# Optimization experiments

Hardware: AMD Instinct MI355X
Metric: run time of the kernel (lower is better)

## Reference

```python
import jax, jax.numpy as jnp
import numpy as np

N = 50000      # nodes
E = 800000     # edges (avg degree 16)
IN = 128       # in_feats
OUT = 128      # out_feats
ASSIGN = 256   # assign_dim = B graphs * 8 clusters
B = 32         # batch_size (num graphs)


def setup_inputs() -> dict:
    key = jax.random.key(0)
    k0, k1, k2, k3 = jax.random.split(key, 4)
    x = jax.random.normal(k0, (N, IN), jnp.float32)
    edge_index = jax.random.randint(k1, (2, E), 0, N, dtype=jnp.int32)
    # sorted graph ids, ~equal-sized graphs (mirrors block_diag mask construction)
    batch = ((jnp.arange(N, dtype=jnp.int32) * B) // N).astype(jnp.int32)
    # SAGEConv params: Linear(2*in_feats -> out) on concat([x, mean_neigh])
    W_embed = jax.random.normal(k2, (2 * IN, OUT), jnp.float32) / np.float32(np.sqrt(2 * IN))
    b_embed = jnp.zeros((OUT,), jnp.float32)
    W_pool = jax.random.normal(k3, (2 * IN, ASSIGN), jnp.float32) / np.float32(np.sqrt(2 * IN))
    b_pool = jnp.zeros((ASSIGN,), jnp.float32)
    return dict(x=x, edge_index=edge_index, batch=batch,
                W_embed=W_embed, b_embed=b_embed, W_pool=W_pool, b_pool=b_pool)


def _sage(x, src, dst, W, b):
    # mean aggregation over in-neighbors (messages src -> dst), then Linear on concat
    n = x.shape[0]
    deg = jax.ops.segment_sum(jnp.ones((src.shape[0],), x.dtype), dst, num_segments=n)
    neigh = jax.ops.segment_sum(x[src], dst, num_segments=n) / jnp.maximum(deg, 1.0)[:, None]
    return jnp.concatenate([x, neigh], axis=-1) @ W + b


def reference(x, edge_index, batch, W_embed, b_embed, W_pool, b_pool):
    src, dst = edge_index[0], edge_index[1]
    embed = _sage(x, src, dst, W_embed, b_embed)                      # [N, OUT]
    pooled = jax.nn.softmax(_sage(x, src, dst, W_pool, b_pool), -1)   # [N, ASSIGN]
    # block-diagonal mask: node i of graph g sees columns [g*C, (g+1)*C)
    C = ASSIGN // B
    cols = jnp.arange(ASSIGN, dtype=batch.dtype) // C
    mask = (batch[:, None] == cols[None, :]).astype(x.dtype)          # [N, ASSIGN]
    # NOTE: faithful to original: softmax of (mask * pooled), zeros contribute exp(0)
    r = jax.nn.softmax(mask * pooled, axis=-1) * mask
    r = r / (r.sum(axis=-1, keepdims=True) + 1e-13)                   # [N, ASSIGN]
    h = r.T @ embed                                                   # [ASSIGN, OUT]
    # adj_new = S^T A S with A sparse COO (rows=edge_index[0], cols=edge_index[1])
    ar = jax.ops.segment_sum(r[dst], src, num_segments=x.shape[0])    # A @ S : [N, ASSIGN]
    adj_new = r.T @ ar                                                # [ASSIGN, ASSIGN]
    return (adj_new, h)
```

## Files before the change

### kernel.cpp

```cpp
#include <hip/hip_runtime.h>
#include <hip/hip_bf16.h>

#define N_ 50000
#define E_ 800000
#define IN_ 128
#define OUT_ 128
#define ASSIGN_ 256
#define B_ 32
#define KTOT 256
#define JTOT 384
#define HCHUNK 32
#define ACHUNK 32
#define AST 72
#define NXP ((N_ + 127) / 128)
#define NGB (NXP * 3)
#define NCVX 6250

#define NBKT 256
#define NPB 196
#define BCAP 4000
#define EPB 4096
#define NBLK_A ((E_ + EPB - 1) / EPB)
#define NPRE (NBLK_A + NCVX + 384)

typedef __attribute__((ext_vector_type(8))) short short8;
typedef __attribute__((ext_vector_type(4))) float f32x4;
typedef __attribute__((ext_vector_type(2))) float f32x2;
typedef __attribute__((ext_vector_type(4))) unsigned short ushort4v;
typedef __attribute__((ext_vector_type(2))) unsigned short ushort2v;
typedef unsigned short u16;

__device__ inline unsigned short f2bf(float v) {
    union { float f; unsigned u; } a;
    a.f = v;
    unsigned r = a.u + 0x7fff + ((a.u >> 16) & 1);
    return (unsigned short)(r >> 16);
}
__device__ inline float bf2f(unsigned short b) {
    union { unsigned u; float f; } a;
    a.u = ((unsigned)b) << 16;
    return a.f;
}

__device__ inline unsigned enc8(float v) {
    union { float f; unsigned u; } a;
    a.f = v * 0x1p-120f;
    unsigned b = a.u;
    unsigned r = b + 0x7FFFF + ((b >> 20) & 1);
    return ((r >> 20) & 0x7F) | ((b >> 24) & 0x80);
}
__device__ inline float2 dec8x2(unsigned short p) {
#if defined(__has_builtin) && __has_builtin(__builtin_amdgcn_cvt_pk_f32_fp8)
    f32x2 r = __builtin_amdgcn_cvt_pk_f32_fp8((int)(unsigned)p, false);
    return make_float2(r.x, r.y);
#else
    unsigned u0 = p & 0xffu, u1 = (p >> 8) & 0xffu;
    union { unsigned u; float f; } a, b;
    a.u = ((u0 & 0x80u) << 24) | ((u0 & 0x7fu) << 20);
    b.u = ((u1 & 0x80u) << 24) | ((u1 & 0x7fu) << 20);
    return make_float2(a.f * 0x1p+120f, b.f * 0x1p+120f);
#endif
}

__global__ __launch_bounds__(256) void k_pre(const int* __restrict__ ei,
                                             int* __restrict__ bktFill,
                                             int2* __restrict__ ebkt,
                                             const float* __restrict__ x,
                                             unsigned short* __restrict__ xhi,
                                             unsigned char* __restrict__ xq,
                                             const float* __restrict__ We,
                                             const float* __restrict__ be,
                                             const float* __restrict__ Wp,
                                             const float* __restrict__ bp,
                                             unsigned short* __restrict__ WThi,
                                             float* __restrict__ bias) {
    __shared__ int lh[NBKT], lbase[NBKT], lofs[NBKT];
    int bid = blockIdx.x;
    int t = threadIdx.x;
    if (bid < NBLK_A) {
        int e0 = bid * EPB;
        lh[t] = 0; lofs[t] = 0;
        __syncthreads();
        int ss[16], dd[16];
#pragma unroll
        for (int i = 0; i < 16; i++) {
            int e = e0 + i * 256 + t;
            ss[i] = 0; dd[i] = -1;
            if (e < E_) {
                ss[i] = ei[e];
                dd[i] = ei[E_ + e];
                atomicAdd(&lh[dd[i] / NPB], 1);
            }
        }
        __syncthreads();
        lbase[t] = t * BCAP + atomicAdd(&bktFill[t], lh[t]);
        __syncthreads();
#pragma unroll
        for (int i = 0; i < 16; i++) {
            if (dd[i] >= 0) {
                int b = dd[i] / NPB;
                int o = atomicAdd(&lofs[b], 1);
                ebkt[lbase[b] + o] = make_int2(ss[i], dd[i]);
            }
        }
        return;
    }
    if (bid >= NBLK_A + NCVX) {
        int idx = (bid - NBLK_A - NCVX) * 256 + t;
        if (idx < JTOT * KTOT) {
            int j = idx / KTOT, k = idx - j * KTOT;
            float v = (j < 128) ? We[k * 128 + j] : Wp[k * 256 + (j - 128)];
            WThi[idx] = f2bf(v);
        }
        if (idx < JTOT) bias[idx] = (idx < 128) ? be[idx] : bp[idx - 128];
        return;
    }
    int i4 = ((bid - NBLK_A) * 256 + t) * 4;
    if (i4 >= N_ * 128) return;
    float4 v = *(const float4*)(x + i4);
    ushort4v h;
    h.x = f2bf(v.x); h.y = f2bf(v.y); h.z = f2bf(v.z); h.w = f2bf(v.w);
    *(ushort4v*)(xhi + i4) = h;
    unsigned q = enc8(v.x) | (enc8(v.y) << 8) | (enc8(v.z) << 16) | (enc8(v.w) << 24);
    *(unsigned*)(xq + i4) = q;
}

__global__ __launch_bounds__(256) void k_binB(const int* __restrict__ bktFill,
                                              const int2* __restrict__ ebkt,
                                              int* __restrict__ ready,
                                              int* __restrict__ rowStart,
                                              int* __restrict__ csr_src,
                                              int* __restrict__ csr_dst) {
    __shared__ int ldeg[NPB];
    __shared__ int lscan[256];
    __shared__ int bsc[NBKT];
    __shared__ int lfill[NPB];
    int b = blockIdx.x, t = threadIdx.x;
    if (t < NPB) ldeg[t] = 0;
    __syncthreads();
    int base = b * BCAP;
    int cnt = bktFill[b];
    int n0 = b * NPB;
    for (int j = t; j < cnt; j += 256)
        atomicAdd(&ldeg[ebkt[base + j].y - n0], 1);
    __syncthreads();
    lscan[t] = (t < NPB) ? ldeg[t] : 0;
    __syncthreads();
    for (int off = 1; off < 256; off <<= 1) {
        int x0 = lscan[t];
        int a0 = (t >= off) ? lscan[t - off] : 0;
        __syncthreads();
        lscan[t] = x0 + a0;
        __syncthreads();
    }
    if (t == 0) atomicExch(&ready[b], lscan[NPB - 1] + 1);
    {
        int v;
        while ((v = atomicAdd(&ready[t], 0)) == 0) __builtin_amdgcn_s_sleep(8);
        bsc[t] = v - 1;
    }
    __syncthreads();
    for (int off = 1; off < NBKT; off <<= 1) {
        int x = bsc[t];
        int add = (t >= off) ? bsc[t - off] : 0;
        __syncthreads();
        bsc[t] = x + add;
        __syncthreads();
    }
    int base0 = (b == 0) ? 0 : bsc[b - 1];
    if (t < NPB) {
        int n = n0 + t;
        if (n < N_) {
            int excl = (t == 0) ? 0 : lscan[t - 1];
            lfill[t] = excl;
            rowStart[n] = base0 + excl;
        }
    }
    __syncthreads();
    for (int j = t; j < cnt; j += 256) {
        int2 sd = ebkt[base + j];
        int p = base0 + atomicAdd(&lfill[sd.y - n0], 1);
        csr_src[p] = sd.x;
        csr_dst[p] = sd.y;
    }
    if (b == 0 && t == 0) rowStart[N_] = E_;
}

__global__ __launch_bounds__(256) void k_agg(const unsigned char* __restrict__ xq,
                                             const int* __restrict__ rowStart,
                                             const int* __restrict__ csr_src,
                                             unsigned short* __restrict__ nhi) {
    int node = blockIdx.x * 4 + (threadIdx.x >> 6);
    if (node >= N_) return;
    int lane = threadIdx.x & 63;
    int es = lane >> 3;
    int fb = lane & 7;
    int a = rowStart[node], bnd = rowStart[node + 1];
    float acc[16];
#pragma unroll
    for (int k = 0; k < 16; k++) acc[k] = 0.f;
#define DEC(Q)                                                       \
    {                                                                \
        unsigned wq[4] = {(Q).x, (Q).y, (Q).z, (Q).w};               \
        _Pragma("unroll")                                            \
        for (int wi = 0; wi < 4; wi++) {                             \
            float2 f01 = dec8x2((unsigned short)(wq[wi] & 0xffffu)); \
            float2 f23 = dec8x2((unsigned short)(wq[wi] >> 16));     \
            acc[wi * 4 + 0] += f01.x; acc[wi * 4 + 1] += f01.y;      \
            acc[wi * 4 + 2] += f23.x; acc[wi * 4 + 3] += f23.y;      \
        }                                                            \
    }
    int j = a;
    for (; j + 8 < bnd; j += 16) {
        int s0 = csr_src[j + es];
        uint4 q0 = *(const uint4*)(xq + (size_t)s0 * 128 + fb * 16);
        uint4 q1 = {0, 0, 0, 0};
        int e1 = j + 8 + es;
        if (e1 < bnd) {
            int s1 = csr_src[e1];
            q1 = *(const uint4*)(xq + (size_t)s1 * 128 + fb * 16);
        }
        DEC(q0);
        DEC(q1);
    }
    if (j < bnd) {
        uint4 q0 = {0, 0, 0, 0};
        int e0 = j + es;
        if (e0 < bnd) {
            int s0 = csr_src[e0];
            q0 = *(const uint4*)(xq + (size_t)s0 * 128 + fb * 16);
        }
        DEC(q0);
    }
#undef DEC
#pragma unroll
    for (int k = 0; k < 16; k++) {
        acc[k] += __shfl_xor(acc[k], 8, 64);
        acc[k] += __shfl_xor(acc[k], 16, 64);
        acc[k] += __shfl_xor(acc[k], 32, 64);
    }
    float inv = 1.0f / (float)max(bnd - a, 1);
    if (es == 0) {
        short8 o0, o1;
#pragma unroll
        for (int k = 0; k < 8; k++) {
            o0[k] = (short)f2bf(acc[k] * inv);
            o1[k] = (short)f2bf(acc[k + 8] * inv);
        }
        *(short8*)(nhi + (size_t)node * 128 + fb * 16) = o0;
        *(short8*)(nhi + (size_t)node * 128 + fb * 16 + 8) = o1;
    }
}

#define LDA 40
__global__ __launch_bounds__(256) void k_gemm(const unsigned short* __restrict__ xhi,
                                              const unsigned short* __restrict__ nhi,
                                              const unsigned short* __restrict__ WThi,
                                              const float* __restrict__ bias,
                                              unsigned short* __restrict__ embed,
                                              unsigned short* __restrict__ plog) {
    __shared__ __align__(16) union {
        struct { u16 Ah[128][LDA]; u16 Bh[128][LDA]; } s;
        u16 ep[64 * 128];
    } sm;
    int t = threadIdx.x;
    int wave = t >> 6, lane = t & 63;
    int wm = wave >> 1, wn = wave & 1;
    int q = lane >> 4, lr = lane & 15;

    int id = blockIdx.x;
    int xi, cc;
    if (id < (NXP / 8) * 24) {
        xi = (id / 24) * 8 + (id & 7);
        cc = (id % 24) >> 3;
    } else {
        int r2 = id - (NXP / 8) * 24;
        xi = (NXP / 8) * 8 + r2 % (NXP % 8);
        cc = r2 / (NXP % 8);
    }
    int row0 = xi * 128;
    int col0 = cc * 128;

    f32x4 acc[4][4] = {};
    int smr = t >> 1;
    int kc = (t & 1) * 16;
    int node = row0 + smr;

    short8 vh0, vh1, wh0, wh1;
#define LOADK(KT)                                                                    \
    {                                                                                \
        const u16* Ah_src = ((KT) < 128) ? xhi : nhi;                                \
        int kb = ((KT) & 127) + kc;                                                  \
        vh0 = {}; vh1 = {};                                                          \
        if (node < N_) {                                                             \
            const short8* ph = (const short8*)(Ah_src + (size_t)node * 128 + kb);    \
            vh0 = ph[0]; vh1 = ph[1];                                                \
        }                                                                            \
        const short8* pw = (const short8*)(WThi + (size_t)(col0 + smr) * 256 + (KT) + kc); \
        wh0 = pw[0]; wh1 = pw[1];                                                    \
    }
    LOADK(0);
    for (int kt = 0; kt < KTOT; kt += 32) {
        *(short8*)&sm.s.Ah[smr][kc] = vh0;
        *(short8*)&sm.s.Ah[smr][kc + 8] = vh1;
        *(short8*)&sm.s.Bh[smr][kc] = wh0;
        *(short8*)&sm.s.Bh[smr][kc + 8] = wh1;
        __syncthreads();
        if (kt + 32 < KTOT) LOADK(kt + 32);

        short8 afh[4];
#pragma unroll
        for (int mi = 0; mi < 4; mi++) {
            int r = wm * 64 + mi * 16 + lr;
            afh[mi] = *(const short8*)&sm.s.Ah[r][q * 8];
        }
#pragma unroll
        for (int ni = 0; ni < 4; ni++) {
            int r = wn * 64 + ni * 16 + lr;
            short8 bfh = *(const short8*)&sm.s.Bh[r][q * 8];
#pragma unroll
            for (int mi = 0; mi < 4; mi++)
                acc[mi][ni] = __builtin_amdgcn_mfma_f32_16x16x32_bf16(afh[mi], bfh, acc[mi][ni], 0, 0, 0);
        }
        __syncthreads();
    }
#undef LOADK

    for (int half = 0; half < 2; half++) {
        __syncthreads();
        if (wm == half) {
#pragma unroll
            for (int mi = 0; mi < 4; mi++)
#pragma unroll
                for (int ni = 0; ni < 4; ni++) {
                    int lcol = wn * 64 + ni * 16 + lr;
                    float bj = bias[col0 + lcol];
#pragma unroll
                    for (int r = 0; r < 4; r++) {
                        int lrow = mi * 16 + q * 4 + r;
                        sm.ep[lrow * 128 + lcol] = f2bf(acc[mi][ni][r] + bj);
                    }
                }
        }
        __syncthreads();
#pragma unroll
        for (int i = 0; i < 4; i++) {
            int chunk = i * 256 + t;
            int lrow = chunk >> 4;
            int lco = (chunk & 15) * 8;
            int grow = row0 + half * 64 + lrow;
            if (grow < N_) {
                short8 v = *(const short8*)&sm.ep[lrow * 128 + lco];
                if (col0 < 128)
                    *(short8*)(embed + (size_t)grow * 128 + lco) = v;
                else
                    *(short8*)(plog + (size_t)grow * 256 + (col0 - 128) + lco) = v;
            }
        }
    }
}

__global__ __launch_bounds__(256) void k_r(const unsigned short* __restrict__ plog,
                                           const int* __restrict__ batch,
                                           float* __restrict__ r8,
                                           unsigned short* __restrict__ r8b) {
    int node = blockIdx.x * 4 + (threadIdx.x >> 6);
    int lane = threadIdx.x & 63;
    if (node >= N_) return;
    ushort4v p4 = *(const ushort4v*)(plog + (size_t)node * 256 + lane * 4);
    float px = bf2f(p4.x), py = bf2f(p4.y), pz = bf2f(p4.z), pw = bf2f(p4.w);
    float m = fmaxf(fmaxf(px, py), fmaxf(pz, pw));
    for (int off = 32; off; off >>= 1) m = fmaxf(m, __shfl_xor(m, off, 64));
    float s = expf(px - m) + expf(py - m) + expf(pz - m) + expf(pw - m);
    for (int off = 32; off; off >>= 1) s += __shfl_xor(s, off, 64);
    int g = batch[node];
    float v = 0.f;
    if (lane < 8) v = expf(bf2f(plog[(size_t)node * 256 + g * 8 + lane]) - m) / s;
    float M2 = v;
    for (int off = 4; off; off >>= 1) M2 = fmaxf(M2, __shfl_xor(M2, off, 64));
    float e = expf(v - M2);
    float Sg = e;
    for (int off = 4; off; off >>= 1) Sg += __shfl_xor(Sg, off, 64);
    float D2 = Sg + 248.0f * expf(-M2);
    float r = e / (Sg + 1e-13f * D2);
    if (lane < 8) {
        r8[node * 8 + lane] = r;
        r8b[node * 8 + lane] = f2bf(r);
    }
}

__global__ __launch_bounds__(256) void k_tail(const int* __restrict__ rowStart,
                                              const int* __restrict__ csr_src,
                                              const int* __restrict__ csr_dst,
                                              const unsigned short* __restrict__ r8b,
                                              float* __restrict__ partAdj,
                                              const unsigned short* __restrict__ embed,
                                              const float* __restrict__ r8,
                                              float* __restrict__ partH) {
    __shared__ __align__(16) unsigned short Ab[256 * AST];
    __shared__ __align__(16) unsigned short Bb[16 * AST];
    int id = blockIdx.x;
    int t = threadIdx.x;
    if (id >= B_ * ACHUNK) {
        int idh = id - B_ * ACHUNK;
        int g = idh & 31;
        int c = idh >> 5;
        int wv = t >> 6, l = t & 63;
        int n0g = (g * N_ + 31) >> 5;
        int n1g = ((g + 1) * N_ + 31) >> 5;
        int len = n1g - n0g;
        int a = n0g + (len * c) / HCHUNK;
        int b = n0g + (len * (c + 1)) / HCHUNK;
        float acc[8][2] = {};
        for (int n = a + wv; n < b; n += 4) {
            unsigned e2 = *(const unsigned*)(embed + (size_t)n * 128 + l * 2);
            float e0 = bf2f((u16)(e2 & 0xffffu));
            float e1 = bf2f((u16)(e2 >> 16));
            f32x4 r0 = *(const f32x4*)(r8 + n * 8);
            f32x4 r1 = *(const f32x4*)(r8 + n * 8 + 4);
#pragma unroll
            for (int c2 = 0; c2 < 4; c2++) {
                acc[c2][0] += r0[c2] * e0; acc[c2][1] += r0[c2] * e1;
                acc[c2 + 4][0] += r1[c2] * e0; acc[c2 + 4][1] += r1[c2] * e1;
            }
        }
        float* hredf = (float*)Ab;
#pragma unroll
        for (int c2 = 0; c2 < 8; c2++) {
            hredf[wv * 1024 + c2 * 128 + l * 2] = acc[c2][0];
            hredf[wv * 1024 + c2 * 128 + l * 2 + 1] = acc[c2][1];
        }
        __syncthreads();
        float* pb = partH + (g * HCHUNK + c) * 1024;
        for (int o = t; o < 1024; o += 256)
            pb[o] = (hredf[o] + hredf[1024 + o]) + (hredf[2048 + o] + hredf[3072 + o]);
        return;
    }
    int gd = id & 31;
    int c = id >> 5;
    int wave = t >> 6, lane = t & 63;
    int q = lane >> 4, lr = lane & 15;
    int n0g = (gd * N_ + 31) >> 5;
    int n1g = ((gd + 1) * N_ + 31) >> 5;
    int len = n1g - n0g;
    int na = n0g + (len * c) / ACHUNK;
    int nb = n0g + (len * (c + 1)) / ACHUNK;
    int j0 = rowStart[na], j1 = rowStart[nb];

    uint4 z = {0, 0, 0, 0};
#pragma unroll
    for (int i = 0; i < 9; i++) *(uint4*)&Ab[(i * 256 + t) * 8] = z;
    if (t < 144) *(uint4*)&Bb[t * 8] = z;
    __syncthreads();

    f32x4 acc[4] = {};
    int el = t >> 2;
    int ap = t & 3;

    int jcur = j0 + el;
    unsigned sv = 0, dv = 0;
    int gs = 0;
    bool have = jcur < j1;
    if (have) {
        int s = csr_src[jcur];
        int d = csr_dst[jcur];
        gs = (s * B_) / N_;
        sv = *(const unsigned*)(r8b + (size_t)s * 8 + ap * 2);
        dv = *(const unsigned*)(r8b + (size_t)d * 8 + ap * 2);
    }
    int pca = -1;

    for (int jt = j0; jt < j1; jt += 64) {
        if (pca >= 0) {
            Ab[pca * AST + el] = 0;
            Ab[(pca + 1) * AST + el] = 0;
            Bb[(ap * 2) * AST + el] = 0;
            Bb[(ap * 2 + 1) * AST + el] = 0;
        }
        int ca = -1;
        if (have) {
            ca = gs * 8 + ap * 2;
            Ab[ca * AST + el] = (unsigned short)sv;
            Ab[(ca + 1) * AST + el] = (unsigned short)(sv >> 16);
            Bb[(ap * 2) * AST + el] = (unsigned short)dv;
            Bb[(ap * 2 + 1) * AST + el] = (unsigned short)(dv >> 16);
        }
        __syncthreads();
        int jn = jt + 64 + el;
        bool haveN = jn < j1;
        unsigned svN = 0, dvN = 0;
        int gsN = 0;
        if (haveN) {
            int s = csr_src[jn];
            int d = csr_dst[jn];
            gsN = (s * B_) / N_;
            svN = *(const unsigned*)(r8b + (size_t)s * 8 + ap * 2);
            dvN = *(const unsigned*)(r8b + (size_t)d * 8 + ap * 2);
        }
        short8 bf0 = *(const short8*)&Bb[lr * AST + q * 8];
        short8 bf1 = *(const short8*)&Bb[lr * AST + 32 + q * 8];
#pragma unroll
        for (int mi = 0; mi < 4; mi++) {
            int col = (wave * 4 + mi) * 16 + lr;
            short8 a0 = *(const short8*)&Ab[col * AST + q * 8];
            short8 a1 = *(const short8*)&Ab[col * AST + 32 + q * 8];
            acc[mi] = __builtin_amdgcn_mfma_f32_16x16x32_bf16(a0, bf0, acc[mi], 0, 0, 0);
            acc[mi] = __builtin_amdgcn_mfma_f32_16x16x32_bf16(a1, bf1, acc[mi], 0, 0, 0);
        }
        __syncthreads();
        pca = ca;
        have = haveN; gs = gsN; sv = svN; dv = dvN;
    }

    float* pb = partAdj + (gd * ACHUNK + c) * 2048;
    if (lr < 8) {
#pragma unroll
        for (int mi = 0; mi < 4; mi++) {
            int mbase = (wave * 4 + mi) * 16 + q * 4;
#pragma unroll
            for (int r = 0; r < 4; r++)
                pb[(mbase + r) * 8 + lr] = acc[mi][r];
        }
    }
}

__global__ __launch_bounds__(256) void k_red(const float* __restrict__ partAdj,
                                             const float* __restrict__ partH,
                                             float* __restrict__ out) {
    int o = blockIdx.x * 256 + threadIdx.x;
    if (o < 256 * 256) {
        int row = o >> 8, col = o & 255;
        int gd = col >> 3, b = col & 7;
        int li = row * 8 + b;
        float s = 0.f;
#pragma unroll
        for (int c = 0; c < ACHUNK; c++) s += partAdj[(gd * ACHUNK + c) * 2048 + li];
        out[o] = s;
    } else {
        int idx = o - 256 * 256;
        int g = idx >> 10;
        int local = idx & 1023;
        float s = 0.f;
#pragma unroll
        for (int c = 0; c < HCHUNK; c++) s += partH[(g * HCHUNK + c) * 1024 + local];
        out[256 * 256 + idx] = s;
    }
}

extern "C" void kernel_launch(void* const* d_in, const int* in_sizes, int n_in,
                              void* d_out, int out_size, void* d_ws, size_t ws_size,
                              hipStream_t stream) {
    const float* x = (const float*)d_in[0];
    const int* ei = (const int*)d_in[1];
    const int* batch = (const int*)d_in[2];
    const float* We = (const float*)d_in[3];
    const float* be = (const float*)d_in[4];
    const float* Wp = (const float*)d_in[5];
    const float* bp = (const float*)d_in[6];
    float* out = (float*)d_out;

    char* w = (char*)d_ws;
    auto alloc = [&](size_t bytes) -> char* {
        char* p = w;
        w += (bytes + 255) & ~(size_t)255;
        return p;
    };
    unsigned short* xhi = (unsigned short*)alloc((size_t)N_ * 128 * 2);
    unsigned char* xq = (unsigned char*)alloc((size_t)N_ * 128);
    unsigned short* nhi = (unsigned short*)alloc((size_t)N_ * 128 * 2);
    unsigned short* WThi = (unsigned short*)alloc((size_t)JTOT * KTOT * 2);
    unsigned short* embed = (unsigned short*)alloc((size_t)N_ * 128 * 2);
    unsigned short* plog = (unsigned short*)alloc((size_t)N_ * 256 * 2);
    float* r8 = (float*)alloc((size_t)N_ * 8 * 4);
    unsigned short* r8b = (unsigned short*)alloc((size_t)N_ * 8 * 2);
    float* bias = (float*)alloc(JTOT * 4);
    int* rowStart = (int*)alloc((size_t)(N_ + 1) * 4);
    int* csr_src = (int*)alloc((size_t)E_ * 4);
    int* csr_dst = (int*)alloc((size_t)E_ * 4);
    int* flags = (int*)alloc(2 * NBKT * 4);
    int* bktFill = flags;
    int* ready = flags + NBKT;
    int2* ebkt = (int2*)alloc((size_t)NBKT * BCAP * 8);
    float* partH = (float*)alloc((size_t)B_ * HCHUNK * 1024 * 4);
    float* partAdj = (float*)alloc((size_t)B_ * ACHUNK * 2048 * 4);

    hipMemsetAsync(flags, 0, 2 * NBKT * 4, stream);
    k_pre<<<NPRE, 256, 0, stream>>>(ei, bktFill, ebkt, x, xhi, xq, We, be, Wp, bp, WThi, bias);
    k_binB<<<NBKT, 256, 0, stream>>>(bktFill, ebkt, ready, rowStart, csr_src, csr_dst);
    k_agg<<<(N_ + 3) / 4, 256, 0, stream>>>(xq, rowStart, csr_src, nhi);
    k_gemm<<<NGB, 256, 0, stream>>>(xhi, nhi, WThi, bias, embed, plog);
    k_r<<<(N_ + 3) / 4, 256, 0, stream>>>(plog, batch, r8, r8b);
    k_tail<<<2 * B_ * ACHUNK, 256, 0, stream>>>(rowStart, csr_src, csr_dst, r8b, partAdj,
                                                embed, r8, partH);
    k_red<<<(256 * 256 + 256 * 128 + 255) / 256, 256, 0, stream>>>(partAdj, partH, out);
}
```

Baseline: 218.0 us.

## Use direct global-to-LDS loads with double-buffered swizzled tiles in GEMM

The GEMM tile staging switches from loading through registers and then storing to padded shared memory, to async global_load_lds 16-byte transfers written straight into LDS. The tiles are double-buffered, so only one barrier per k-step is needed. The padded layout is replaced by an XOR swizzle to avoid bank conflicts. Out-of-range rows are clamped to the last node instead of zero-filled, and the change relies on the barrier waiting for the async loads to complete.

```diff
diff --git a/kernel.cpp b/kernel.cpp
--- a/kernel.cpp
+++ b/kernel.cpp
@@ -60,6 +60,12 @@
     b.u = ((u1 & 0x80u) << 24) | ((u1 & 0x7fu) << 20);
     return make_float2(a.f * 0x1p+120f, b.f * 0x1p+120f);
 #endif
+}
+
+__device__ __forceinline__ void gload16(const u16* g, u16* l) {
+    __builtin_amdgcn_global_load_lds(
+        (const __attribute__((address_space(1))) void*)g,
+        (__attribute__((address_space(3))) void*)l, 16, 0, 0);
 }
 
 __global__ __launch_bounds__(256) void k_pre(const int* __restrict__ ei,
@@ -252,7 +258,6 @@
     }
 }
 
-#define LDA 40
 __global__ __launch_bounds__(256) void k_gemm(const unsigned short* __restrict__ xhi,
                                               const unsigned short* __restrict__ nhi,
                                               const unsigned short* __restrict__ WThi,
@@ -260,7 +265,7 @@
                                               unsigned short* __restrict__ embed,
                                               unsigned short* __restrict__ plog) {
     __shared__ __align__(16) union {
-        struct { u16 Ah[128][LDA]; u16 Bh[128][LDA]; } s;
+        struct { u16 A[2][128 * 32]; u16 B[2][128 * 32]; } s;
         u16 ep[64 * 128];
     } sm;
     int t = threadIdx.x;
@@ -282,49 +287,52 @@
     int col0 = cc * 128;
 
     f32x4 acc[4][4] = {};
-    int smr = t >> 1;
-    int kc = (t & 1) * 16;
-    int node = row0 + smr;
-
-    short8 vh0, vh1, wh0, wh1;
-#define LOADK(KT)                                                                    \
+
+    int segRow[2], segSl[2];
+#pragma unroll
+    for (int i = 0; i < 2; i++) {
+        int R0 = (wave * 2 + i) * 16;
+        segRow[i] = R0 + (lane >> 2);
+        segSl[i] = (lane & 3) ^ ((segRow[i] >> 1) & 3);
+    }
+
+#define ISSUE(KT, BUF)                                                               \
     {                                                                                \
-        const u16* Ah_src = ((KT) < 128) ? xhi : nhi;                                \
-        int kb = ((KT) & 127) + kc;                                                  \
-        vh0 = {}; vh1 = {};                                                          \
-        if (node < N_) {                                                             \
-            const short8* ph = (const short8*)(Ah_src + (size_t)node * 128 + kb);    \
-            vh0 = ph[0]; vh1 = ph[1];                                                \
+        const u16* Asrc = ((KT) < 128) ? xhi : nhi;                                  \
+        int kb = (KT) & 127;                                                         \
+        _Pragma("unroll")                                                            \
+        for (int i = 0; i < 2; i++) {                                                \
+            int nd = row0 + segRow[i];                                               \
+            if (nd >= N_) nd = N_ - 1;                                               \
+            gload16(Asrc + (size_t)nd * 128 + kb + segSl[i] * 8,                     \
+                    &sm.s.A[BUF][((wave * 2 + i) * 16) * 32] + lane * 8);            \
+            gload16(WThi + (size_t)(col0 + segRow[i]) * 256 + (KT) + segSl[i] * 8,   \
+                    &sm.s.B[BUF][((wave * 2 + i) * 16) * 32] + lane * 8);            \
         }                                                                            \
-        const short8* pw = (const short8*)(WThi + (size_t)(col0 + smr) * 256 + (KT) + kc); \
-        wh0 = pw[0]; wh1 = pw[1];                                                    \
-    }
-    LOADK(0);
-    for (int kt = 0; kt < KTOT; kt += 32) {
-        *(short8*)&sm.s.Ah[smr][kc] = vh0;
-        *(short8*)&sm.s.Ah[smr][kc + 8] = vh1;
-        *(short8*)&sm.s.Bh[smr][kc] = wh0;
-        *(short8*)&sm.s.Bh[smr][kc + 8] = wh1;
-        __syncthreads();
-        if (kt + 32 < KTOT) LOADK(kt + 32);
+    }
+
+    ISSUE(0, 0);
+    int p = 0;
+    for (int kt = 0; kt < KTOT; kt += 32, p ^= 1) {
+        __syncthreads();
+        if (kt + 32 < KTOT) ISSUE(kt + 32, p ^ 1);
 
         short8 afh[4];
 #pragma unroll
         for (int mi = 0; mi < 4; mi++) {
             int r = wm * 64 + mi * 16 + lr;
-            afh[mi] = *(const short8*)&sm.s.Ah[r][q * 8];
+            afh[mi] = *(const short8*)&sm.s.A[p][r * 32 + ((q * 8) ^ (((r >> 1) & 3) * 8))];
         }
 #pragma unroll
         for (int ni = 0; ni < 4; ni++) {
             int r = wn * 64 + ni * 16 + lr;
-            short8 bfh = *(const short8*)&sm.s.Bh[r][q * 8];
+            short8 bfh = *(const short8*)&sm.s.B[p][r * 32 + ((q * 8) ^ (((r >> 1) & 3) * 8))];
 #pragma unroll
             for (int mi = 0; mi < 4; mi++)
                 acc[mi][ni] = __builtin_amdgcn_mfma_f32_16x16x32_bf16(afh[mi], bfh, acc[mi][ni], 0, 0, 0);
         }
-        __syncthreads();
-    }
-#undef LOADK
+    }
+#undef ISSUE
 
     for (int half = 0; half < 2; half++) {
         __syncthreads();
```

New measurement: 213.2 us (median of 2 runs). 1.02x faster.
